# Performance work log

Hardware: AMD Instinct MI355X
Metric: run time of the kernel (lower is better)

The kernel has to match this reference:

```python
import jax, jax.numpy as jnp
import numpy as np

SIGMA = 0.5          # init kwarg sigma
PATCH = 5            # init kwarg patch_size
TILE = 32            # init kwarg patch_distance (tile side)
H_PARAM = (PATCH // 2) ** 0.5  # self.h = sqrt(patch_size//2)


def _nlm(tiles, sigma, p, Hp):
    # tiles: [b, c, h, w] -- faithful jax port of nlm()
    b, c, h, w = tiles.shape
    pad = p // 2
    padded = jnp.pad(tiles, ((0, 0), (0, 0), (pad, pad), (pad, pad)), mode='edge')  # replicate pad
    # unfold: all p*p shifted views -> [b, c, p*p, h, w] (channel-major then patch index,
    # matching torch unfold + unflatten(1, (c, p*p)))
    pats = jnp.stack([padded[:, :, i:i + h, j:j + w]
                      for i in range(p) for j in range(p)], axis=2)
    center = p * p // 2
    keep = np.array([k for k in range(p * p) if k != center])
    N = h * w
    d = c * (p * p - 1)
    yN = pats[:, :, keep].reshape(b, d, N).transpose(0, 2, 1)  # [b, N, d]
    # pairwise euclidean distance (cdist)
    sq = jnp.sum(yN * yN, axis=-1)  # [b, N]
    d2 = sq[:, :, None] + sq[:, None, :] - 2.0 * jnp.einsum('bnd,bmd->bnm', yN, yN)
    dist = jnp.sqrt(jnp.maximum(d2, 0.0))  # [b, N, N]
    density = jnp.exp(-dist / (2.0 * Hp ** 2 * sigma ** 2))
    # diag set to +inf in dist -> density diag = 0
    density = density * (1.0 - jnp.eye(N, dtype=density.dtype))
    weight = density / jnp.sum(density, axis=-1, keepdims=True)  # [b, N, N]
    y = tiles.reshape(b, c, N)  # [b, c, N]
    mmse = jnp.einsum('bnm,bcm->bcn', weight, y)  # weighted sum of pixel values
    return mmse.reshape(b, c, h, w)


def reference(image):
    # Tile image into non-overlapping TILE x TILE tiles, run nlm batched, fold back.
    b, c, h, w = image.shape
    T = TILE
    nh, nw = h // T, w // T
    tiles = image.reshape(b, c, nh, T, nw, T).transpose(0, 2, 4, 1, 3, 5)
    tiles = tiles.reshape(b * nh * nw, c, T, T)
    out = _nlm(tiles, SIGMA, PATCH, H_PARAM)
    out = out.reshape(b, nh, nw, c, T, T).transpose(0, 3, 1, 4, 2, 5)
    return out.reshape(b, c, h, w)


def setup_inputs() -> dict:
    key = jax.random.key(0)
    image = jax.random.uniform(key, (1, 3, 320, 320), dtype=jnp.float32)
    return {"image": image}
```

## Files before the change

### kernel.cpp

```cpp
#include <hip/hip_runtime.h>
#include <math.h>

#define TS   32
#define PT   36
#define NPIX 1024
#define DF   72
#define KP   96
#define IMH  320
#define IMW  320
#define NTW  10
#define NTILE 100

#define F_UNITS_PER_TILE 12288
#define FHI_BYTES (NTILE * F_UNITS_PER_TILE * 16)
#define SQ_OFF    (2 * FHI_BYTES)

#define K2LOG2E 2.0813689810056077f

typedef __attribute__((ext_vector_type(8))) short bf16x8;
typedef __attribute__((ext_vector_type(8))) unsigned short u16x8;
typedef __attribute__((ext_vector_type(4))) float f32x4;
typedef __attribute__((ext_vector_type(4))) __fp16 f16x4;
typedef __attribute__((ext_vector_type(2))) __fp16 f16x2;

__global__ __launch_bounds__(256)
void nlm_feat_kernel(const float* __restrict__ img,
                     u16x8* __restrict__ Fhi, float* __restrict__ Sq)
{
    __shared__ float Ploc[3][6][36];
    __shared__ int   ofsl[KP];
    const int tid  = threadIdx.x;
    const int part = blockIdx.x;
    const int tile = blockIdx.y;
    const int by   = (tile / NTW) * TS;
    const int bx   = (tile % NTW) * TS;
    const float* Pf = &Ploc[0][0][0];

    for (int idx = tid; idx < 3 * 6 * 36; idx += 256) {
        int c   = idx / 216;
        int rem = idx - c * 216;
        int yl  = rem / 36;
        int x   = rem - yl * 36;
        int y   = 2 * part + yl;
        int iy  = min(max(y - 2, 0), TS - 1);
        int ix  = min(max(x - 2, 0), TS - 1);
        Ploc[c][yl][x] = img[(c * IMH + by + iy) * IMW + bx + ix];
    }
    if (tid < KP) {
        int k = tid, v = 0;
        if (k < DF) {
            int c = k / 24, o = k - c * 24;
            int kk = o + (o >= 12);
            int i = kk / 5, j = kk - (kk / 5) * 5;
            v = c * 216 + i * 36 + j;
        }
        ofsl[k] = v;
    }
    __syncthreads();

    if (tid < 64) {
        int m  = part * 64 + tid;
        int my = m >> 5, mx = m & 31;
        int ly0 = my - 2 * part;
        float s = 0.f;
        #pragma unroll
        for (int k = 0; k < 25; ++k) {
            if (k == 12) continue;
            int i = k / 5, j = k - (k / 5) * 5;
            float v0 = Ploc[0][ly0 + i][mx + j];
            float v1 = Ploc[1][ly0 + i][mx + j];
            float v2 = Ploc[2][ly0 + i][mx + j];
            s = fmaf(v0, v0, s); s = fmaf(v1, v1, s); s = fmaf(v2, v2, s);
        }
        Sq[tile * NPIX + m] = s * K2LOG2E;
    }

    #pragma unroll
    for (int q = 0; q < 3; ++q) {
        int u    = part * 768 + q * 256 + tid;
        int row  = u & 15;
        int c4   = (u >> 4) & 3;
        int rks  = u >> 6;
        int ks   = rks - (rks / 3) * 3;
        int rt   = rks / 3;
        int r    = rt * 16 + row;
        int lbase = ((r >> 5) - 2 * part) * 36 + (r & 31);
        u16x8 h;
        #pragma unroll
        for (int j = 0; j < 8; ++j) {
            int k = ks * 32 + c4 * 8 + j;
            unsigned short hs = 0;
            if (k < DF) {
                float f = Pf[lbase + ofsl[k]];
                unsigned int uu = __float_as_uint(f);
                hs = (unsigned short)((uu + 0x7fffu + ((uu >> 16) & 1u)) >> 16);
            }
            h[j] = hs;
        }
        Fhi[tile * F_UNITS_PER_TILE + u] = h;
    }
}

__global__ __launch_bounds__(256)
__attribute__((amdgpu_waves_per_eu(4, 8)))
void nlm_gemm_kernel(const float* __restrict__ img,
                     const bf16x8* __restrict__ Fhi,
                     const float* __restrict__ SqK, float* __restrict__ out)
{
    __shared__ __fp16 Yhi[4][1032];
    __shared__ __fp16 Ylo[4][1032];
    __shared__ float red[4][2][16][4];

    const int tid  = threadIdx.x;
    const int lane = tid & 63;
    const int wv   = tid >> 6;
    const int i0   = blockIdx.x;
    const int w    = (i0 & 7) * 400 + (i0 >> 3);
    const int tile = w >> 5;
    const int rtA  = (w & 31) * 2;
    const int by   = (tile / NTW) * TS;
    const int bx   = (tile % NTW) * TS;
    const int quad = lane >> 4;
    const int col  = lane & 15;
    const int ycol = col & 3;

    const bf16x8* FHt = Fhi + tile * F_UNITS_PER_TILE;
    const float*  Sqt = SqK + tile * NPIX;

    for (int idx = tid; idx < 1024; idx += 256) {
        int c = idx >> 8, m4 = (idx & 255) << 2;
        f32x4 v = {1.f, 1.f, 1.f, 1.f};
        if (c < 3) v = *(const f32x4*)&img[(c * IMH + by + (m4 >> 5)) * IMW + bx + (m4 & 31)];
        f16x4 h, l;
        #pragma unroll
        for (int j = 0; j < 4; ++j) {
            h[j] = (__fp16)v[j];
            l[j] = (__fp16)(v[j] - (float)h[j]);
        }
        *(f16x4*)&Yhi[c][m4] = h;
        *(f16x4*)&Ylo[c][m4] = l;
    }

    bf16x8 bN[2][3];
    #pragma unroll
    for (int t = 0; t < 2; ++t)
        #pragma unroll
        for (int ks = 0; ks < 3; ++ks)
            bN[t][ks] = FHt[((rtA + t) * 3 + ks) * 64 + lane];
    asm volatile(""
        : "+v"(bN[0][0]), "+v"(bN[0][1]), "+v"(bN[0][2]),
          "+v"(bN[1][0]), "+v"(bN[1][1]), "+v"(bN[1][2]));

    float snK[2];
    #pragma unroll
    for (int t = 0; t < 2; ++t)
        snK[t] = Sqt[(rtA + t) * 16 + col];

    f32x4 DpvH0 = {0.f, 0.f, 0.f, 0.f};
    f32x4 DpvL0 = {0.f, 0.f, 0.f, 0.f};
    f32x4 DpvH1 = {0.f, 0.f, 0.f, 0.f};
    f32x4 DpvL1 = {0.f, 0.f, 0.f, 0.f};

    __syncthreads();

    const int mtBase = wv * 16;

    bf16x8 aFA0, aFA1, aFA2, aFB0, aFB1, aFB2;
    f32x4 sqA, sqB;
    f16x4 bhiA, bloA, bhiB, bloB;

#define LOADF(mt, a0, a1, a2, sq, bh, bl)                      \
    do {                                                       \
        int _mt = (mt);                                        \
        a0 = FHt[(_mt * 3 + 0) * 64 + lane];                   \
        a1 = FHt[(_mt * 3 + 1) * 64 + lane];                   \
        a2 = FHt[(_mt * 3 + 2) * 64 + lane];                   \
        sq = *(const f32x4*)&Sqt[_mt * 16 + quad * 4];         \
        bh = *(const f16x4*)&Yhi[ycol][_mt * 16 + quad * 4];   \
        bl = *(const f16x4*)&Ylo[ycol][_mt * 16 + quad * 4];   \
    } while (0)

#define COMPUTE(mt, a0, a1, a2, sq, bh, bl)                                          \
    do {                                                                             \
        int _mt = (mt);                                                              \
        f32x4 C0 = {0.f, 0.f, 0.f, 0.f};                                             \
        f32x4 C1 = {0.f, 0.f, 0.f, 0.f};                                             \
        C0 = __builtin_amdgcn_mfma_f32_16x16x32_bf16(a0, bN[0][0], C0, 0, 0, 0);     \
        C1 = __builtin_amdgcn_mfma_f32_16x16x32_bf16(a0, bN[1][0], C1, 0, 0, 0);     \
        C0 = __builtin_amdgcn_mfma_f32_16x16x32_bf16(a1, bN[0][1], C0, 0, 0, 0);     \
        C1 = __builtin_amdgcn_mfma_f32_16x16x32_bf16(a1, bN[1][1], C1, 0, 0, 0);     \
        C0 = __builtin_amdgcn_mfma_f32_16x16x32_bf16(a2, bN[0][2], C0, 0, 0, 0);     \
        C1 = __builtin_amdgcn_mfma_f32_16x16x32_bf16(a2, bN[1][2], C1, 0, 0, 0);     \
        _Pragma("unroll")                                                            \
        for (int t = 0; t < 2; ++t) {                                                \
            f32x4 C = t ? C1 : C0;                                                   \
            float d[4];                                                              \
            _Pragma("unroll")                                                        \
            for (int i = 0; i < 4; ++i) {                                            \
                float s2 = fmaxf(fmaf(-2.0f * K2LOG2E, C[i], sq[i] + snK[t]), 0.f);  \
                d[i] = __builtin_amdgcn_exp2f(-__builtin_amdgcn_sqrtf(s2));          \
            }                                                                        \
            if (_mt == rtA + t) {                                                    \
                _Pragma("unroll")                                                    \
                for (int i = 0; i < 4; ++i)                                          \
                    if (quad * 4 + i == col) d[i] = 0.f;                             \
            }                                                                        \
            f16x2 p0 = __builtin_amdgcn_cvt_pkrtz(d[0], d[1]);                       \
            f16x2 p1 = __builtin_amdgcn_cvt_pkrtz(d[2], d[3]);                       \
            f16x4 wp = __builtin_shufflevector(p0, p1, 0, 1, 2, 3);                  \
            if (t == 0) {                                                            \
                DpvH0 = __builtin_amdgcn_mfma_f32_16x16x16f16(wp, bh, DpvH0, 0, 0, 0); \
                DpvL0 = __builtin_amdgcn_mfma_f32_16x16x16f16(wp, bl, DpvL0, 0, 0, 0); \
            } else {                                                                 \
                DpvH1 = __builtin_amdgcn_mfma_f32_16x16x16f16(wp, bh, DpvH1, 0, 0, 0); \
                DpvL1 = __builtin_amdgcn_mfma_f32_16x16x16f16(wp, bl, DpvL1, 0, 0, 0); \
            }                                                                        \
        }                                                                            \
    } while (0)

    LOADF(mtBase, aFA0, aFA1, aFA2, sqA, bhiA, bloA);
    #pragma unroll
    for (int it2 = 0; it2 < 8; ++it2) {
        const int mt0 = mtBase + it2 * 2;
        LOADF(mt0 + 1, aFB0, aFB1, aFB2, sqB, bhiB, bloB);
        COMPUTE(mt0, aFA0, aFA1, aFA2, sqA, bhiA, bloA);
        if (it2 < 7)
            LOADF(mt0 + 2, aFA0, aFA1, aFA2, sqA, bhiA, bloA);
        COMPUTE(mt0 + 1, aFB0, aFB1, aFB2, sqB, bhiB, bloB);
    }
#undef LOADF
#undef COMPUTE

    if (col < 4) {
        #pragma unroll
        for (int i = 0; i < 4; ++i) {
            red[wv][0][quad * 4 + i][col] = DpvH0[i] + DpvL0[i];
            red[wv][1][quad * 4 + i][col] = DpvH1[i] + DpvL1[i];
        }
    }
    __syncthreads();

    if (tid < 128) {
        int n = tid >> 2, c = tid & 3;
        int t = n >> 4, r = n & 15;
        float s = red[0][t][r][c] + red[1][t][r][c]
                + red[2][t][r][c] + red[3][t][r][c];
        float rs = __shfl(s, (tid & 63) | 3, 64);
        if (c < 3) {
            int nn = rtA * 16 + n;
            int gy = by + (nn >> 5), gx = bx + (nn & 31);
            out[(c * IMH + gy) * IMW + gx] = s * (1.0f / rs);
        }
    }
}

extern "C" void kernel_launch(void* const* d_in, const int* in_sizes, int n_in,
                              void* d_out, int out_size, void* d_ws, size_t ws_size,
                              hipStream_t stream) {
    const float* img = (const float*)d_in[0];
    float* out = (float*)d_out;
    char* ws = (char*)d_ws;
    u16x8* Fhi = (u16x8*)ws;
    float* Sq  = (float*)(ws + SQ_OFF);

    dim3 fgrid(16, NTILE);
    nlm_feat_kernel<<<fgrid, 256, 0, stream>>>(img, Fhi, Sq);
    nlm_gemm_kernel<<<dim3(3200), 256, 0, stream>>>(img, (const bf16x8*)Fhi, Sq, out);
}
```

Before: 111.1 us.

## Split each block's column range across eight waves with a three-stage load pipeline

The GEMM kernel now launches 512 threads per block, so eight waves each process 8 column tiles instead of four waves processing 16. The aim is a shorter serial loop per wave and more latency hiding. The double-buffered register prefetch becomes a three-slot ring that loads two tiles ahead. The cross-wave reduction grows to eight partial sums, which adds shared memory and reduction work, and the extra waves and prefetch slots raise register pressure.

```diff
diff --git a/kernel.cpp b/kernel.cpp
--- a/kernel.cpp
+++ b/kernel.cpp
@@ -101,7 +101,7 @@
     }
 }
 
-__global__ __launch_bounds__(256)
+__global__ __launch_bounds__(512)
 __attribute__((amdgpu_waves_per_eu(4, 8)))
 void nlm_gemm_kernel(const float* __restrict__ img,
                      const bf16x8* __restrict__ Fhi,
@@ -109,7 +109,7 @@
 {
     __shared__ __fp16 Yhi[4][1032];
     __shared__ __fp16 Ylo[4][1032];
-    __shared__ float red[4][2][16][4];
+    __shared__ float red[8][2][16][4];
 
     const int tid  = threadIdx.x;
     const int lane = tid & 63;
@@ -127,7 +127,7 @@
     const bf16x8* FHt = Fhi + tile * F_UNITS_PER_TILE;
     const float*  Sqt = SqK + tile * NPIX;
 
-    for (int idx = tid; idx < 1024; idx += 256) {
+    for (int idx = tid; idx < 1024; idx += 512) {
         int c = idx >> 8, m4 = (idx & 255) << 2;
         f32x4 v = {1.f, 1.f, 1.f, 1.f};
         if (c < 3) v = *(const f32x4*)&img[(c * IMH + by + (m4 >> 5)) * IMW + bx + (m4 & 31)];
@@ -163,41 +163,41 @@
 
     __syncthreads();
 
-    const int mtBase = wv * 16;
-
-    bf16x8 aFA0, aFA1, aFA2, aFB0, aFB1, aFB2;
-    f32x4 sqA, sqB;
-    f16x4 bhiA, bloA, bhiB, bloB;
-
-#define LOADF(mt, a0, a1, a2, sq, bh, bl)                      \
-    do {                                                       \
-        int _mt = (mt);                                        \
-        a0 = FHt[(_mt * 3 + 0) * 64 + lane];                   \
-        a1 = FHt[(_mt * 3 + 1) * 64 + lane];                   \
-        a2 = FHt[(_mt * 3 + 2) * 64 + lane];                   \
-        sq = *(const f32x4*)&Sqt[_mt * 16 + quad * 4];         \
-        bh = *(const f16x4*)&Yhi[ycol][_mt * 16 + quad * 4];   \
-        bl = *(const f16x4*)&Ylo[ycol][_mt * 16 + quad * 4];   \
+    const int mtBase = wv * 8;
+
+    bf16x8 aS[3][3];
+    f32x4  sqS[3];
+    f16x4  bhS[3], blS[3];
+
+#define LOADF(mt_, si)                                          \
+    do {                                                        \
+        int _mt = (mt_);                                        \
+        aS[si][0] = FHt[(_mt * 3 + 0) * 64 + lane];             \
+        aS[si][1] = FHt[(_mt * 3 + 1) * 64 + lane];             \
+        aS[si][2] = FHt[(_mt * 3 + 2) * 64 + lane];             \
+        sqS[si] = *(const f32x4*)&Sqt[_mt * 16 + quad * 4];     \
+        bhS[si] = *(const f16x4*)&Yhi[ycol][_mt * 16 + quad * 4]; \
+        blS[si] = *(const f16x4*)&Ylo[ycol][_mt * 16 + quad * 4]; \
     } while (0)
 
-#define COMPUTE(mt, a0, a1, a2, sq, bh, bl)                                          \
+#define COMPUTE(mt_, si)                                                             \
     do {                                                                             \
-        int _mt = (mt);                                                              \
+        int _mt = (mt_);                                                             \
         f32x4 C0 = {0.f, 0.f, 0.f, 0.f};                                             \
         f32x4 C1 = {0.f, 0.f, 0.f, 0.f};                                             \
-        C0 = __builtin_amdgcn_mfma_f32_16x16x32_bf16(a0, bN[0][0], C0, 0, 0, 0);     \
-        C1 = __builtin_amdgcn_mfma_f32_16x16x32_bf16(a0, bN[1][0], C1, 0, 0, 0);     \
-        C0 = __builtin_amdgcn_mfma_f32_16x16x32_bf16(a1, bN[0][1], C0, 0, 0, 0);     \
-        C1 = __builtin_amdgcn_mfma_f32_16x16x32_bf16(a1, bN[1][1], C1, 0, 0, 0);     \
-        C0 = __builtin_amdgcn_mfma_f32_16x16x32_bf16(a2, bN[0][2], C0, 0, 0, 0);     \
-        C1 = __builtin_amdgcn_mfma_f32_16x16x32_bf16(a2, bN[1][2], C1, 0, 0, 0);     \
+        C0 = __builtin_amdgcn_mfma_f32_16x16x32_bf16(aS[si][0], bN[0][0], C0, 0, 0, 0); \
+        C1 = __builtin_amdgcn_mfma_f32_16x16x32_bf16(aS[si][0], bN[1][0], C1, 0, 0, 0); \
+        C0 = __builtin_amdgcn_mfma_f32_16x16x32_bf16(aS[si][1], bN[0][1], C0, 0, 0, 0); \
+        C1 = __builtin_amdgcn_mfma_f32_16x16x32_bf16(aS[si][1], bN[1][1], C1, 0, 0, 0); \
+        C0 = __builtin_amdgcn_mfma_f32_16x16x32_bf16(aS[si][2], bN[0][2], C0, 0, 0, 0); \
+        C1 = __builtin_amdgcn_mfma_f32_16x16x32_bf16(aS[si][2], bN[1][2], C1, 0, 0, 0); \
         _Pragma("unroll")                                                            \
         for (int t = 0; t < 2; ++t) {                                                \
             f32x4 C = t ? C1 : C0;                                                   \
             float d[4];                                                              \
             _Pragma("unroll")                                                        \
             for (int i = 0; i < 4; ++i) {                                            \
-                float s2 = fmaxf(fmaf(-2.0f * K2LOG2E, C[i], sq[i] + snK[t]), 0.f);  \
+                float s2 = fmaxf(fmaf(-2.0f * K2LOG2E, C[i], sqS[si][i] + snK[t]), 0.f); \
                 d[i] = __builtin_amdgcn_exp2f(-__builtin_amdgcn_sqrtf(s2));          \
             }                                                                        \
             if (_mt == rtA + t) {                                                    \
@@ -209,24 +209,21 @@
             f16x2 p1 = __builtin_amdgcn_cvt_pkrtz(d[2], d[3]);                       \
             f16x4 wp = __builtin_shufflevector(p0, p1, 0, 1, 2, 3);                  \
             if (t == 0) {                                                            \
-                DpvH0 = __builtin_amdgcn_mfma_f32_16x16x16f16(wp, bh, DpvH0, 0, 0, 0); \
-                DpvL0 = __builtin_amdgcn_mfma_f32_16x16x16f16(wp, bl, DpvL0, 0, 0, 0); \
+                DpvH0 = __builtin_amdgcn_mfma_f32_16x16x16f16(wp, bhS[si], DpvH0, 0, 0, 0); \
+                DpvL0 = __builtin_amdgcn_mfma_f32_16x16x16f16(wp, blS[si], DpvL0, 0, 0, 0); \
             } else {                                                                 \
-                DpvH1 = __builtin_amdgcn_mfma_f32_16x16x16f16(wp, bh, DpvH1, 0, 0, 0); \
-                DpvL1 = __builtin_amdgcn_mfma_f32_16x16x16f16(wp, bl, DpvL1, 0, 0, 0); \
+                DpvH1 = __builtin_amdgcn_mfma_f32_16x16x16f16(wp, bhS[si], DpvH1, 0, 0, 0); \
+                DpvL1 = __builtin_amdgcn_mfma_f32_16x16x16f16(wp, blS[si], DpvL1, 0, 0, 0); \
             }                                                                        \
         }                                                                            \
     } while (0)
 
-    LOADF(mtBase, aFA0, aFA1, aFA2, sqA, bhiA, bloA);
-    #pragma unroll
-    for (int it2 = 0; it2 < 8; ++it2) {
-        const int mt0 = mtBase + it2 * 2;
-        LOADF(mt0 + 1, aFB0, aFB1, aFB2, sqB, bhiB, bloB);
-        COMPUTE(mt0, aFA0, aFA1, aFA2, sqA, bhiA, bloA);
-        if (it2 < 7)
-            LOADF(mt0 + 2, aFA0, aFA1, aFA2, sqA, bhiA, bloA);
-        COMPUTE(mt0 + 1, aFB0, aFB1, aFB2, sqB, bhiB, bloB);
+    LOADF(mtBase + 0, 0);
+    LOADF(mtBase + 1, 1);
+    #pragma unroll
+    for (int it = 0; it < 8; ++it) {
+        if (it + 2 < 8) LOADF(mtBase + it + 2, (it + 2) % 3);
+        COMPUTE(mtBase + it, it % 3);
     }
 #undef LOADF
 #undef COMPUTE
@@ -243,8 +240,10 @@
     if (tid < 128) {
         int n = tid >> 2, c = tid & 3;
         int t = n >> 4, r = n & 15;
-        float s = red[0][t][r][c] + red[1][t][r][c]
-                + red[2][t][r][c] + red[3][t][r][c];
+        float s = 0.f;
+        #pragma unroll
+        for (int ww = 0; ww < 8; ++ww)
+            s += red[ww][t][r][c];
         float rs = __shfl(s, (tid & 63) | 3, 64);
         if (c < 3) {
             int nn = rtA * 16 + n;
@@ -265,5 +264,5 @@
 
     dim3 fgrid(16, NTILE);
     nlm_feat_kernel<<<fgrid, 256, 0, stream>>>(img, Fhi, Sq);
-    nlm_gemm_kernel<<<dim3(3200), 256, 0, stream>>>(img, (const bf16x8*)Fhi, Sq, out);
+    nlm_gemm_kernel<<<dim3(3200), 512, 0, stream>>>(img, (const bf16x8*)Fhi, Sq, out);
 }
```

Result: slower. 114.0 us (+2.6%).

## Exploit distance-matrix symmetry with triangular tiles and a partial-sum reduction pass

Applied to the files above, without the earlier changes.

The pairwise-distance kernel now computes only the upper triangle of 16x16 row-tile pairs per image tile, so each exp/sqrt evaluation is used twice. The transposed contribution goes through an identity-matrix MFMA and LDS atomics into a per-block accumulator. Per-strip partial sums are written to workspace, and a new reduce kernel sums them and normalizes. A scale factor is folded into the bf16 features and the sign is flipped on B, so the MFMA accumulator yields the scaled squared distance directly. The cost is extra MFMAs and LDS atomics, triangular load imbalance across waves, a third kernel launch, and roughly 26 MB of partial-sum traffic through workspace.

```diff
diff --git a/kernel.cpp b/kernel.cpp
--- a/kernel.cpp
+++ b/kernel.cpp
@@ -2,7 +2,6 @@
 #include <math.h>
 
 #define TS   32
-#define PT   36
 #define NPIX 1024
 #define DF   72
 #define KP   96
@@ -10,12 +9,15 @@
 #define IMW  320
 #define NTW  10
 #define NTILE 100
+#define STRIPS 16
 
 #define F_UNITS_PER_TILE 12288
 #define FHI_BYTES (NTILE * F_UNITS_PER_TILE * 16)
 #define SQ_OFF    (2 * FHI_BYTES)
+#define PART_OFF  (64u << 20)
 
 #define K2LOG2E 2.0813689810056077f
+#define FSCALE  2.0402789f
 
 typedef __attribute__((ext_vector_type(8))) short bf16x8;
 typedef __attribute__((ext_vector_type(8))) unsigned short u16x8;
@@ -91,7 +93,7 @@
             int k = ks * 32 + c4 * 8 + j;
             unsigned short hs = 0;
             if (k < DF) {
-                float f = Pf[lbase + ofsl[k]];
+                float f = Pf[lbase + ofsl[k]] * FSCALE;
                 unsigned int uu = __float_as_uint(f);
                 hs = (unsigned short)((uu + 0x7fffu + ((uu >> 16) & 1u)) >> 16);
             }
@@ -103,29 +105,36 @@
 
 __global__ __launch_bounds__(256)
 __attribute__((amdgpu_waves_per_eu(4, 8)))
-void nlm_gemm_kernel(const float* __restrict__ img,
-                     const bf16x8* __restrict__ Fhi,
-                     const float* __restrict__ SqK, float* __restrict__ out)
+void nlm_sym_kernel(const float* __restrict__ img,
+                    const bf16x8* __restrict__ Fhi,
+                    const float* __restrict__ SqK,
+                    float* __restrict__ part)
 {
     __shared__ __fp16 Yhi[4][1032];
     __shared__ __fp16 Ylo[4][1032];
-    __shared__ float red[4][2][16][4];
+    __shared__ float acc[NPIX][4];
+
+    const int x    = blockIdx.x & 7;
+    const int r    = blockIdx.x >> 3;
+    const int k    = r / 13;
+    const int tile = x + 8 * (r - k * 13);
+    if (tile >= NTILE) return;
 
     const int tid  = threadIdx.x;
     const int lane = tid & 63;
     const int wv   = tid >> 6;
-    const int i0   = blockIdx.x;
-    const int w    = (i0 & 7) * 400 + (i0 >> 3);
-    const int tile = w >> 5;
-    const int rtA  = (w & 31) * 2;
-    const int by   = (tile / NTW) * TS;
-    const int bx   = (tile % NTW) * TS;
     const int quad = lane >> 4;
     const int col  = lane & 15;
     const int ycol = col & 3;
+    const int iw   = k * 4 + wv;
+    const int by   = (tile / NTW) * TS;
+    const int bx   = (tile % NTW) * TS;
 
     const bf16x8* FHt = Fhi + tile * F_UNITS_PER_TILE;
     const float*  Sqt = SqK + tile * NPIX;
+
+    for (int idx = tid; idx < 4096; idx += 256)
+        ((float*)acc)[idx] = 0.f;
 
     for (int idx = tid; idx < 1024; idx += 256) {
         int c = idx >> 8, m4 = (idx & 255) << 2;
@@ -141,117 +150,130 @@
         *(f16x4*)&Ylo[c][m4] = l;
     }
 
-    bf16x8 bN[2][3];
+    bf16x8 bN0, bN1, bN2;
+    {
+        bf16x8 sgn;
+        #pragma unroll
+        for (int j = 0; j < 8; ++j) sgn[j] = (short)0x8000;
+        bN0 = FHt[(iw * 3 + 0) * 64 + lane] ^ sgn;
+        bN1 = FHt[(iw * 3 + 1) * 64 + lane] ^ sgn;
+        bN2 = FHt[(iw * 3 + 2) * 64 + lane] ^ sgn;
+    }
+    asm volatile("" : "+v"(bN0), "+v"(bN1), "+v"(bN2));
+    const float sni = Sqt[iw * 16 + col];
+    f16x4 idf;
     #pragma unroll
-    for (int t = 0; t < 2; ++t)
-        #pragma unroll
-        for (int ks = 0; ks < 3; ++ks)
-            bN[t][ks] = FHt[((rtA + t) * 3 + ks) * 64 + lane];
-    asm volatile(""
-        : "+v"(bN[0][0]), "+v"(bN[0][1]), "+v"(bN[0][2]),
-          "+v"(bN[1][0]), "+v"(bN[1][1]), "+v"(bN[1][2]));
-
-    float snK[2];
-    #pragma unroll
-    for (int t = 0; t < 2; ++t)
-        snK[t] = Sqt[(rtA + t) * 16 + col];
-
-    f32x4 DpvH0 = {0.f, 0.f, 0.f, 0.f};
-    f32x4 DpvL0 = {0.f, 0.f, 0.f, 0.f};
-    f32x4 DpvH1 = {0.f, 0.f, 0.f, 0.f};
-    f32x4 DpvL1 = {0.f, 0.f, 0.f, 0.f};
-
-    __syncthreads();
-
-    const int mtBase = wv * 16;
-
-    bf16x8 aFA0, aFA1, aFA2, aFB0, aFB1, aFB2;
-    f32x4 sqA, sqB;
-    f16x4 bhiA, bloA, bhiB, bloB;
-
-#define LOADF(mt, a0, a1, a2, sq, bh, bl)                      \
-    do {                                                       \
-        int _mt = (mt);                                        \
-        a0 = FHt[(_mt * 3 + 0) * 64 + lane];                   \
-        a1 = FHt[(_mt * 3 + 1) * 64 + lane];                   \
-        a2 = FHt[(_mt * 3 + 2) * 64 + lane];                   \
-        sq = *(const f32x4*)&Sqt[_mt * 16 + quad * 4];         \
-        bh = *(const f16x4*)&Yhi[ycol][_mt * 16 + quad * 4];   \
-        bl = *(const f16x4*)&Ylo[ycol][_mt * 16 + quad * 4];   \
+    for (int j = 0; j < 4; ++j)
+        idf[j] = (__fp16)((quad * 4 + j == col) ? 1.f : 0.f);
+
+    f32x4 Dn = {0.f, 0.f, 0.f, 0.f};
+
+    __syncthreads();
+
+    const f16x4 bhN = *(const f16x4*)&Yhi[ycol][iw * 16 + quad * 4];
+    const f16x4 blN = *(const f16x4*)&Ylo[ycol][iw * 16 + quad * 4];
+
+#define LOADJ(j_, a0, a1, a2, sq, bh, bl)                        \
+    do {                                                         \
+        int _j = (j_);                                           \
+        a0 = FHt[(_j * 3 + 0) * 64 + lane];                      \
+        a1 = FHt[(_j * 3 + 1) * 64 + lane];                      \
+        a2 = FHt[(_j * 3 + 2) * 64 + lane];                      \
+        sq = *(const f32x4*)&Sqt[_j * 16 + quad * 4];            \
+        bh = *(const f16x4*)&Yhi[ycol][_j * 16 + quad * 4];      \
+        bl = *(const f16x4*)&Ylo[ycol][_j * 16 + quad * 4];      \
     } while (0)
 
-#define COMPUTE(mt, a0, a1, a2, sq, bh, bl)                                          \
+#define COMPUTEJ(j_, a0, a1, a2, sq, bh, bl)                                         \
     do {                                                                             \
-        int _mt = (mt);                                                              \
-        f32x4 C0 = {0.f, 0.f, 0.f, 0.f};                                             \
-        f32x4 C1 = {0.f, 0.f, 0.f, 0.f};                                             \
-        C0 = __builtin_amdgcn_mfma_f32_16x16x32_bf16(a0, bN[0][0], C0, 0, 0, 0);     \
-        C1 = __builtin_amdgcn_mfma_f32_16x16x32_bf16(a0, bN[1][0], C1, 0, 0, 0);     \
-        C0 = __builtin_amdgcn_mfma_f32_16x16x32_bf16(a1, bN[0][1], C0, 0, 0, 0);     \
-        C1 = __builtin_amdgcn_mfma_f32_16x16x32_bf16(a1, bN[1][1], C1, 0, 0, 0);     \
-        C0 = __builtin_amdgcn_mfma_f32_16x16x32_bf16(a2, bN[0][2], C0, 0, 0, 0);     \
-        C1 = __builtin_amdgcn_mfma_f32_16x16x32_bf16(a2, bN[1][2], C1, 0, 0, 0);     \
+        int _j = (j_);                                                               \
+        f32x4 C = {sq[0] + sni, sq[1] + sni, sq[2] + sni, sq[3] + sni};              \
+        C = __builtin_amdgcn_mfma_f32_16x16x32_bf16(a0, bN0, C, 0, 0, 0);            \
+        C = __builtin_amdgcn_mfma_f32_16x16x32_bf16(a1, bN1, C, 0, 0, 0);            \
+        C = __builtin_amdgcn_mfma_f32_16x16x32_bf16(a2, bN2, C, 0, 0, 0);            \
+        float d[4];                                                                  \
         _Pragma("unroll")                                                            \
-        for (int t = 0; t < 2; ++t) {                                                \
-            f32x4 C = t ? C1 : C0;                                                   \
-            float d[4];                                                              \
+        for (int i = 0; i < 4; ++i) {                                                \
+            float s2 = fmaxf(C[i], 0.f);                                             \
+            d[i] = __builtin_amdgcn_exp2f(-__builtin_amdgcn_sqrtf(s2));              \
+        }                                                                            \
+        if (_j == iw) {                                                              \
             _Pragma("unroll")                                                        \
-            for (int i = 0; i < 4; ++i) {                                            \
-                float s2 = fmaxf(fmaf(-2.0f * K2LOG2E, C[i], sq[i] + snK[t]), 0.f);  \
-                d[i] = __builtin_amdgcn_exp2f(-__builtin_amdgcn_sqrtf(s2));          \
-            }                                                                        \
-            if (_mt == rtA + t) {                                                    \
-                _Pragma("unroll")                                                    \
-                for (int i = 0; i < 4; ++i)                                          \
-                    if (quad * 4 + i == col) d[i] = 0.f;                             \
-            }                                                                        \
-            f16x2 p0 = __builtin_amdgcn_cvt_pkrtz(d[0], d[1]);                       \
-            f16x2 p1 = __builtin_amdgcn_cvt_pkrtz(d[2], d[3]);                       \
-            f16x4 wp = __builtin_shufflevector(p0, p1, 0, 1, 2, 3);                  \
-            if (t == 0) {                                                            \
-                DpvH0 = __builtin_amdgcn_mfma_f32_16x16x16f16(wp, bh, DpvH0, 0, 0, 0); \
-                DpvL0 = __builtin_amdgcn_mfma_f32_16x16x16f16(wp, bl, DpvL0, 0, 0, 0); \
-            } else {                                                                 \
-                DpvH1 = __builtin_amdgcn_mfma_f32_16x16x16f16(wp, bh, DpvH1, 0, 0, 0); \
-                DpvL1 = __builtin_amdgcn_mfma_f32_16x16x16f16(wp, bl, DpvL1, 0, 0, 0); \
+            for (int i = 0; i < 4; ++i)                                              \
+                if (quad * 4 + i == col) d[i] = 0.f;                                 \
+        }                                                                            \
+        f16x2 p0 = __builtin_amdgcn_cvt_pkrtz(d[0], d[1]);                           \
+        f16x2 p1 = __builtin_amdgcn_cvt_pkrtz(d[2], d[3]);                           \
+        f16x4 wp = __builtin_shufflevector(p0, p1, 0, 1, 2, 3);                      \
+        Dn = __builtin_amdgcn_mfma_f32_16x16x16f16(wp, bh, Dn, 0, 0, 0);             \
+        Dn = __builtin_amdgcn_mfma_f32_16x16x16f16(wp, bl, Dn, 0, 0, 0);             \
+        if (_j != iw) {                                                              \
+            f32x4 Z = {0.f, 0.f, 0.f, 0.f};                                          \
+            f32x4 T = __builtin_amdgcn_mfma_f32_16x16x16f16(wp, idf, Z, 0, 0, 0);    \
+            f16x2 q0 = __builtin_amdgcn_cvt_pkrtz(T[0], T[1]);                       \
+            f16x2 q1 = __builtin_amdgcn_cvt_pkrtz(T[2], T[3]);                       \
+            f16x4 wq = __builtin_shufflevector(q0, q1, 0, 1, 2, 3);                  \
+            f32x4 D2 = __builtin_amdgcn_mfma_f32_16x16x16f16(wq, bhN, Z, 0, 0, 0);   \
+            D2 = __builtin_amdgcn_mfma_f32_16x16x16f16(wq, blN, D2, 0, 0, 0);        \
+            if (col < 4) {                                                           \
+                atomicAdd(&acc[_j * 16 + quad * 4 + 0][col], D2[0]);                 \
+                atomicAdd(&acc[_j * 16 + quad * 4 + 1][col], D2[1]);                 \
+                atomicAdd(&acc[_j * 16 + quad * 4 + 2][col], D2[2]);                 \
+                atomicAdd(&acc[_j * 16 + quad * 4 + 3][col], D2[3]);                 \
             }                                                                        \
         }                                                                            \
     } while (0)
 
-    LOADF(mtBase, aFA0, aFA1, aFA2, sqA, bhiA, bloA);
+    bf16x8 aA0, aA1, aA2, aB0, aB1, aB2;
+    f32x4 sqA, sqB;
+    f16x4 bhA, blA, bhB, blB;
+
+    int j = iw;
+    LOADJ(j, aA0, aA1, aA2, sqA, bhA, blA);
+    while (j + 1 < 64) {
+        LOADJ(j + 1, aB0, aB1, aB2, sqB, bhB, blB);
+        COMPUTEJ(j, aA0, aA1, aA2, sqA, bhA, blA);
+        if (j + 2 < 64) LOADJ(j + 2, aA0, aA1, aA2, sqA, bhA, blA);
+        COMPUTEJ(j + 1, aB0, aB1, aB2, sqB, bhB, blB);
+        j += 2;
+    }
+    if (j < 64) COMPUTEJ(j, aA0, aA1, aA2, sqA, bhA, blA);
+#undef LOADJ
+#undef COMPUTEJ
+
+    __syncthreads();
+
+    if (col < 4) {
+        #pragma unroll
+        for (int s = 0; s < 4; ++s)
+            acc[iw * 16 + quad * 4 + s][col] += Dn[s];
+    }
+    __syncthreads();
+
+    float* P = part + (size_t)(tile * STRIPS + k) * (NPIX * 4);
+    for (int idx = tid; idx < 4096; idx += 256)
+        P[idx] = ((float*)acc)[idx];
+}
+
+__global__ __launch_bounds__(256)
+void nlm_reduce_kernel(const float* __restrict__ part, float* __restrict__ out)
+{
+    const int bid  = blockIdx.x;
+    const int tile = bid >> 2;
+    const int p    = ((bid & 3) << 8) + threadIdx.x;
+    const float* base = part + (size_t)tile * (STRIPS * NPIX * 4) + p * 4;
+    float s0 = 0.f, s1 = 0.f, s2 = 0.f, s3 = 0.f;
     #pragma unroll
-    for (int it2 = 0; it2 < 8; ++it2) {
-        const int mt0 = mtBase + it2 * 2;
-        LOADF(mt0 + 1, aFB0, aFB1, aFB2, sqB, bhiB, bloB);
-        COMPUTE(mt0, aFA0, aFA1, aFA2, sqA, bhiA, bloA);
-        if (it2 < 7)
-            LOADF(mt0 + 2, aFA0, aFA1, aFA2, sqA, bhiA, bloA);
-        COMPUTE(mt0 + 1, aFB0, aFB1, aFB2, sqB, bhiB, bloB);
-    }
-#undef LOADF
-#undef COMPUTE
-
-    if (col < 4) {
-        #pragma unroll
-        for (int i = 0; i < 4; ++i) {
-            red[wv][0][quad * 4 + i][col] = DpvH0[i] + DpvL0[i];
-            red[wv][1][quad * 4 + i][col] = DpvH1[i] + DpvL1[i];
-        }
-    }
-    __syncthreads();
-
-    if (tid < 128) {
-        int n = tid >> 2, c = tid & 3;
-        int t = n >> 4, r = n & 15;
-        float s = red[0][t][r][c] + red[1][t][r][c]
-                + red[2][t][r][c] + red[3][t][r][c];
-        float rs = __shfl(s, (tid & 63) | 3, 64);
-        if (c < 3) {
-            int nn = rtA * 16 + n;
-            int gy = by + (nn >> 5), gx = bx + (nn & 31);
-            out[(c * IMH + gy) * IMW + gx] = s * (1.0f / rs);
-        }
-    }
+    for (int st = 0; st < STRIPS; ++st) {
+        f32x4 v = *(const f32x4*)(base + st * (NPIX * 4));
+        s0 += v[0]; s1 += v[1]; s2 += v[2]; s3 += v[3];
+    }
+    float inv = 1.f / s3;
+    int by = (tile / NTW) * TS, bx = (tile % NTW) * TS;
+    int gy = by + (p >> 5), gx = bx + (p & 31);
+    out[(0 * IMH + gy) * IMW + gx] = s0 * inv;
+    out[(1 * IMH + gy) * IMW + gx] = s1 * inv;
+    out[(2 * IMH + gy) * IMW + gx] = s2 * inv;
 }
 
 extern "C" void kernel_launch(void* const* d_in, const int* in_sizes, int n_in,
@@ -262,8 +284,10 @@
     char* ws = (char*)d_ws;
     u16x8* Fhi = (u16x8*)ws;
     float* Sq  = (float*)(ws + SQ_OFF);
+    float* prt = (float*)(ws + PART_OFF);
 
     dim3 fgrid(16, NTILE);
     nlm_feat_kernel<<<fgrid, 256, 0, stream>>>(img, Fhi, Sq);
-    nlm_gemm_kernel<<<dim3(3200), 256, 0, stream>>>(img, (const bf16x8*)Fhi, Sq, out);
-}
+    nlm_sym_kernel<<<dim3(1664), 256, 0, stream>>>(img, (const bf16x8*)Fhi, Sq, prt);
+    nlm_reduce_kernel<<<dim3(400), 256, 0, stream>>>(prt, out);
+}
```

New measurement: 145.5 us. 1.31x slower.
